# Performance work log

Hardware: AMD Instinct MI355X
Metric: run time of the kernel (lower is better)

The kernel has to match this reference:

```python
import jax, jax.numpy as jnp
import numpy as np

N_HEADS = 16
D_K = 64
MAX_LEN = 5000


def setup_inputs() -> dict:
    key = jax.random.key(0)
    ks = jax.random.split(key, 6)
    B, L, D = 4, 1024, 1024
    s = 1.0 / np.sqrt(D).astype(np.float32)
    return {
        "x": jax.random.normal(ks[0], (B, L, D), jnp.float32),
        "W_q": jax.random.normal(ks[1], (D, D), jnp.float32) * s,
        "b_q": jnp.zeros((D,), jnp.float32),
        "W_k": jax.random.normal(ks[2], (D, D), jnp.float32) * s,
        "b_k": jnp.zeros((D,), jnp.float32),
        "W_v": jax.random.normal(ks[3], (D, D), jnp.float32) * s,
        "b_v": jnp.zeros((D,), jnp.float32),
        "W_o": jax.random.normal(ks[4], (D, D), jnp.float32) * s,
        "b_o": jnp.zeros((D,), jnp.float32),
        "Er": jax.random.normal(ks[5], (MAX_LEN, D_K), jnp.float32) * 0.02,
    }


def reference(x, W_q, b_q, W_k, b_k, W_v, b_v, W_o, b_o, Er):
    B, L, D = x.shape
    H = N_HEADS
    dk = D // H
    # torch nn.Linear: y = x @ W.T + b
    Q = (x @ W_q.T + b_q).reshape(B, L, H, dk).transpose(0, 2, 1, 3)  # (B,H,L,dk)
    K = (x @ W_k.T + b_k).reshape(B, L, H, dk).transpose(0, 2, 1, 3)
    V = (x @ W_v.T + b_v).reshape(B, L, H, dk).transpose(0, 2, 1, 3)
    AC = jnp.einsum('bhid,bhjd->bhij', Q, K)  # (B,H,L,L)
    rel_pos = jnp.arange(L - 1, -L, -1) + (MAX_LEN - 1)  # (2L-1,)
    # mode='clip' matches intended math: clamped rows fall in the part that
    # the relative shift slices away.
    Er_embed = jnp.take(Er, rel_pos, axis=0, mode='clip')  # (2L-1, dk)
    BD = jnp.einsum('bhid,rd->bhir', Q, Er_embed)  # (B,H,L,2L-1)
    # _relative_shift: view is a no-op (shape already (B,H,L,2L-1)), then slice
    BD = BD[..., L - 1:]  # (B,H,L,L)
    scores = (AC + BD) / np.sqrt(dk).astype(np.float32)
    attn = jax.nn.softmax(scores, axis=-1)
    out = jnp.einsum('bhij,bhjd->bhid', attn, V)
    out = out.transpose(0, 2, 1, 3).reshape(B, L, D)
    return out @ W_o.T + b_o
```

## Files before the change

### kernel.cpp

```cpp
#include <hip/hip_runtime.h>
#include <cstdint>
#include <cstddef>


typedef __attribute__((ext_vector_type(8))) short short8;
typedef __attribute__((ext_vector_type(4))) float f32x4;

#define MFMA_BF16(a, b, c) __builtin_amdgcn_mfma_f32_16x16x32_bf16((a), (b), (c), 0, 0, 0)

constexpr int kB = 4, kL = 1024, kD = 1024, kH = 16;
constexpr int kBL = kB * kL;
constexpr float kScale = 0.125f * 1.44269504088896340736f;

static __device__ __forceinline__ unsigned short f32_to_bf16(float f) {
  union { float f; uint32_t u; } c; c.f = f;
  uint32_t u = c.u + 0x7fffu + ((c.u >> 16) & 1u);
  return (unsigned short)(u >> 16);
}

static __device__ __forceinline__ void gload_lds16(const void* g, void* l) {
  __builtin_amdgcn_global_load_lds(
      (const __attribute__((address_space(1))) void*)g,
      (__attribute__((address_space(3))) void*)l, 16, 0, 0);
}

__global__ __launch_bounds__(256)
void cast_all(const float* __restrict__ x,  const float* __restrict__ Wq,
              const float* __restrict__ Wk, const float* __restrict__ Wv,
              const float* __restrict__ Wo,
              unsigned short* __restrict__ xb, unsigned short* __restrict__ Wcat,
              unsigned short* __restrict__ Wob) {
  int i = blockIdx.x * blockDim.x + threadIdx.x;
  const float* src;
  ushort4* dst;
  int off;
  if (i < 1048576) {
    src = x; dst = reinterpret_cast<ushort4*>(xb); off = i;
  } else {
    int j = i - 1048576;
    int seg = j >> 18;
    off = j & 262143;
    if (seg == 0)      { src = Wq; dst = reinterpret_cast<ushort4*>(Wcat); }
    else if (seg == 1) { src = Wk; dst = reinterpret_cast<ushort4*>(Wcat) + 262144; }
    else if (seg == 2) { src = Wv; dst = reinterpret_cast<ushort4*>(Wcat) + 524288; }
    else               { src = Wo; dst = reinterpret_cast<ushort4*>(Wob); }
  }
  float4 v = reinterpret_cast<const float4*>(src)[off];
  ushort4 o;
  o.x = f32_to_bf16(v.x); o.y = f32_to_bf16(v.y);
  o.z = f32_to_bf16(v.z); o.w = f32_to_bf16(v.w);
  dst[off] = o;
}

__global__ __launch_bounds__(512, 2)
void gemm_qkv(const unsigned short* __restrict__ A,
              const unsigned short* __restrict__ Bm,
              const float* __restrict__ bq, const float* __restrict__ bk,
              const float* __restrict__ bv,
              const float* __restrict__ Er,
              unsigned short* __restrict__ Qh, unsigned short* __restrict__ Kh,
              unsigned short* __restrict__ Vth) {
  __shared__ __align__(16) char smem[131072];
  const int tid  = threadIdx.x;
  const int lane = tid & 63, wave = tid >> 6;
  const int quad = lane >> 4, l15 = lane & 15, lhalf = l15 >> 1;
  const int wr = wave >> 2, wc = wave & 3;

  const int bid = blockIdx.x;
  const int xcd = bid & 7, idx = bid >> 3;
  const int mt_ = idx / 6, nt_ = idx - mt_ * 6;
  const int m0 = ((xcd >> 1) * 4 + mt_) * 256;
  const int n0 = ((xcd & 1) * 6 + nt_) * 256;

  const int lane_off = (l15 & 1) * 64 + ((quad * 16) ^ ((lhalf & 3) << 4));
  const int aoff = lhalf * 128 + lane_off + wr * 8192;
  const int boff = lhalf * 128 + lane_off + wc * 4096;

  int srow[2], scol[2];
#pragma unroll
  for (int j = 0; j < 2; ++j) {
    int poff = (j * 512 + tid) * 16;
    int L = poff ^ (((poff >> 7) & 3) << 4);
    srow[j] = ((L >> 7) << 1) | ((L >> 6) & 1);
    scol[j] = (L & 63) >> 1;
  }

  auto stageAB = [&](int X, int kh, int tt) {
    const unsigned short* src = X ? Bm : A;
    const int rbase = X ? n0 : m0;
    char* dst = smem + ((tt & 1) * 65536 + X * 32768 + kh * 16384) + tid * 16;
    const int kc = tt * 64 + kh * 32;
#pragma unroll
    for (int j = 0; j < 2; ++j)
      gload_lds16(src + (size_t)(rbase + srow[j]) * 1024 + kc + scol[j],
                  dst + j * 8192);
  };

  const f32x4 vzero = {0.f, 0.f, 0.f, 0.f};
  f32x4 acc[8][4];
#pragma unroll
  for (int i = 0; i < 8; ++i)
#pragma unroll
    for (int j = 0; j < 4; ++j) acc[i][j] = vzero;

  stageAB(0, 0, 0); stageAB(1, 0, 0); stageAB(0, 1, 0); stageAB(1, 1, 0);
  stageAB(0, 0, 1); stageAB(1, 0, 1);
  asm volatile("s_waitcnt vmcnt(4)" ::: "memory");
  __builtin_amdgcn_s_barrier();

#define LDA(KH, MB) do {                                                      \
    _Pragma("unroll")                                                         \
    for (int f_ = 0; f_ < 4; ++f_)                                            \
      af[f_] = *(const short8*)(RA + (KH) * 16384 + aoff + ((MB) + f_) * 1024); \
  } while (0)
#define LDB(KH) do {                                                          \
    _Pragma("unroll")                                                         \
    for (int n_ = 0; n_ < 4; ++n_)                                            \
      bf[n_] = *(const short8*)(RB + (KH) * 16384 + boff + n_ * 1024);        \
  } while (0)
#define BARA() do {                                                           \
    __builtin_amdgcn_s_barrier();                                             \
    asm volatile("s_waitcnt lgkmcnt(0)" ::: "memory");                        \
    __builtin_amdgcn_sched_barrier(0);                                        \
  } while (0)
#define MFMA_QUAD(MB) do {                                                    \
    __builtin_amdgcn_s_setprio(1);                                            \
    _Pragma("unroll")                                                         \
    for (int mq_ = 0; mq_ < 4; ++mq_) {                                       \
      _Pragma("unroll")                                                       \
      for (int nq_ = 0; nq_ < 4; ++nq_)                                       \
        acc[(MB) + mq_][nq_] =                                                \
            MFMA_BF16(af[mq_], bf[nq_], acc[(MB) + mq_][nq_]);                \
    }                                                                         \
    __builtin_amdgcn_s_setprio(0);                                            \
  } while (0)

  for (int t = 0; t < 16; ++t) {
    const char* RA = smem + (t & 1) * 65536;
    const char* RB = RA + 32768;
    short8 af[4], bf[4];
    LDA(0, 0); LDB(0);
    if (t + 1 < 16) stageAB(0, 1, t + 1);
    BARA(); MFMA_QUAD(0);
    __builtin_amdgcn_s_barrier();
    LDA(0, 4);
    if (t + 1 < 16) stageAB(1, 1, t + 1);
    BARA(); MFMA_QUAD(4);
    __builtin_amdgcn_s_barrier();
    LDA(1, 0); LDB(1);
    if (t + 2 < 16) stageAB(0, 0, t + 2);
    BARA(); MFMA_QUAD(0);
    __builtin_amdgcn_s_barrier();
    LDA(1, 4);
    if (t + 2 < 16) stageAB(1, 0, t + 2);
    BARA(); MFMA_QUAD(4);
    if (t < 14) asm volatile("s_waitcnt vmcnt(4)" ::: "memory");
    else        asm volatile("s_waitcnt vmcnt(0)" ::: "memory");
    __builtin_amdgcn_s_barrier();
  }

#undef LDA
#undef LDB
#undef BARA
#undef MFMA_QUAD

  const int wsel = n0 >> 10;
  const int gmb  = m0 + wr * 128;
  const int bb   = gmb >> 10, i0l = gmb & 1023;
  const int nl0  = (n0 & 1023) + wc * 64;
  const int hh   = nl0 >> 6;
  const size_t bh = (size_t)(bb * 16 + hh);

  if (wsel == 0) {
#pragma unroll
    for (int mf = 0; mf < 8; ++mf)
#pragma unroll
      for (int nf = 0; nf < 4; ++nf)
#pragma unroll
        for (int r = 0; r < 4; ++r) {
          const int i = i0l + mf * 16 + quad * 4 + r;
          const int n = nl0 + nf * 16 + l15;
          float v = (acc[mf][nf][r] + bq[n]) * kScale;
          Qh[(bh * 1024 + i) * 64 + (n & 63)] = f32_to_bf16(v);
        }
  } else if (wsel == 1) {
#pragma unroll
    for (int mf = 0; mf < 8; ++mf)
#pragma unroll
      for (int nf = 0; nf < 4; ++nf)
#pragma unroll
        for (int r = 0; r < 4; ++r) {
          const int i = i0l + mf * 16 + quad * 4 + r;
          const int n = nl0 + nf * 16 + l15;
          const int d = n & 63;
          float v = acc[mf][nf][r] + bk[n] + Er[(size_t)(4999 - i) * 64 + d];
          Kh[(bh * 1024 + i) * 64 + d] = f32_to_bf16(v);
        }
  } else {
    __syncthreads();
    unsigned short* W = (unsigned short*)smem + (size_t)wave * 8192;
#pragma unroll
    for (int mf = 0; mf < 8; ++mf)
#pragma unroll
      for (int nf = 0; nf < 4; ++nf) {
        ushort4 pk;
        const int n = nl0 + nf * 16 + l15;
        pk.x = f32_to_bf16(acc[mf][nf][0] + bv[n]);
        pk.y = f32_to_bf16(acc[mf][nf][1] + bv[n]);
        pk.z = f32_to_bf16(acc[mf][nf][2] + bv[n]);
        pk.w = f32_to_bf16(acc[mf][nf][3] + bv[n]);
        *(ushort4*)&W[(size_t)(nf * 16 + l15) * 128 + mf * 16 + quad * 4] = pk;
      }
#pragma unroll
    for (int p = 0; p < 16; ++p) {
      const int u = p * 64 + lane;
      const int d = u >> 4, ch = (u & 15) * 8;
      short8 vv = *(const short8*)&W[(size_t)d * 128 + ch];
      *(short8*)&Vth[(bh * 64 + d) * 1024 + i0l + ch] = vv;
    }
  }
}

__global__ __launch_bounds__(256)
void gemm_out(const unsigned short* __restrict__ A,
              const unsigned short* __restrict__ Bm,
              const float* __restrict__ bias,
              float* __restrict__ outf) {
  __shared__ unsigned short As[2][128 * 32];
  __shared__ unsigned short Bs[2][64 * 32];
  const int tid  = threadIdx.x;
  const int lane = tid & 63, wave = tid >> 6;
  const int quad = lane >> 4, l15 = lane & 15;
  const int m0 = blockIdx.y * 128, n0 = blockIdx.x * 64;
  const int K = 1024;

  const f32x4 vzero = {0.f, 0.f, 0.f, 0.f};
  f32x4 acc[2][4];
#pragma unroll
  for (int i = 0; i < 2; ++i)
#pragma unroll
    for (int j = 0; j < 4; ++j) acc[i][j] = vzero;

  for (int k0 = 0; k0 < K; k0 += 64) {
    __syncthreads();
#pragma unroll
    for (int j = 0; j < 4; ++j) {
      int u = j * 256 + tid;
      int half = u >> 9, row = (u >> 2) & 127, c = (u & 3) * 8 + half * 32;
      gload_lds16(A + (size_t)(m0 + row) * K + k0 + c, (char*)&As[0][0] + (size_t)u * 16);
    }
#pragma unroll
    for (int j = 0; j < 2; ++j) {
      int u = j * 256 + tid;
      int half = u >> 8, row = (u >> 2) & 63, c = (u & 3) * 8 + half * 32;
      gload_lds16(Bm + (size_t)(n0 + row) * K + k0 + c, (char*)&Bs[0][0] + (size_t)u * 16);
    }
    __syncthreads();

#pragma unroll
    for (int ks = 0; ks < 2; ++ks) {
      short8 af[2], bfv[4];
#pragma unroll
      for (int mt = 0; mt < 2; ++mt)
        af[mt] = *(const short8*)&As[ks][(wave * 32 + mt * 16 + l15) * 32 + quad * 8];
#pragma unroll
      for (int nt = 0; nt < 4; ++nt)
        bfv[nt] = *(const short8*)&Bs[ks][(nt * 16 + l15) * 32 + quad * 8];
#pragma unroll
      for (int mt = 0; mt < 2; ++mt)
#pragma unroll
        for (int nt = 0; nt < 4; ++nt)
          acc[mt][nt] = MFMA_BF16(af[mt], bfv[nt], acc[mt][nt]);
    }
  }

#pragma unroll
  for (int mt = 0; mt < 2; ++mt)
#pragma unroll
    for (int nt = 0; nt < 4; ++nt)
#pragma unroll
      for (int r = 0; r < 4; ++r) {
        const int gm = m0 + wave * 32 + mt * 16 + quad * 4 + r;
        const int gn = n0 + nt * 16 + l15;
        outf[(size_t)gm * 1024 + gn] = acc[mt][nt][r] + bias[gn];
      }
}

__global__ __launch_bounds__(256)
void attn_kernel(const unsigned short* __restrict__ Q,
                 const unsigned short* __restrict__ Kp,
                 const unsigned short* __restrict__ Vt,
                 unsigned short* __restrict__ Ao) {
  __shared__ unsigned short Ks[2][2][64 * 32];
  __shared__ unsigned short Vs[2][2][64 * 32];
  __shared__ unsigned short Plds[4][32 * 72];
  const int tid  = threadIdx.x;
  const int lane = tid & 63, wave = tid >> 6;
  const int quad = lane >> 4, l15 = lane & 15;
  const int bh = blockIdx.x;
  const int qb = blockIdx.y;
  const size_t base  = (size_t)bh * (kL * 64);
  const size_t vbase = (size_t)bh * (64 * kL);
  const int i0 = qb * 128 + wave * 32;

  short8 qf[2][2];
#pragma unroll
  for (int mt = 0; mt < 2; ++mt)
#pragma unroll
    for (int ks = 0; ks < 2; ++ks)
      qf[mt][ks] = *(const short8*)
          &Q[base + (size_t)(i0 + mt * 16 + l15) * 64 + ks * 32 + quad * 8];

  auto stage = [&](int buf, int kb) {
#pragma unroll
    for (int j = 0; j < 2; ++j) {
      int u = j * 256 + tid;
      int half = u >> 8, row = (u >> 2) & 63, c = (u & 3) * 8;
      gload_lds16(Kp + base + (size_t)(kb * 64 + row) * 64 + half * 32 + c,
                  (char*)&Ks[buf][0][0] + (size_t)u * 16);
      gload_lds16(Vt + vbase + (size_t)row * kL + kb * 64 + half * 32 + c,
                  (char*)&Vs[buf][0][0] + (size_t)u * 16);
    }
  };

  const f32x4 vzero = {0.f, 0.f, 0.f, 0.f};
  f32x4 of[2][4];
#pragma unroll
  for (int mt = 0; mt < 2; ++mt)
#pragma unroll
    for (int dt = 0; dt < 4; ++dt) of[mt][dt] = vzero;
  float lsum[2][4] = {{0.f, 0.f, 0.f, 0.f}, {0.f, 0.f, 0.f, 0.f}};

  unsigned short* Pw = Plds[wave];

  stage(0, 0);
  __syncthreads();

  for (int kb = 0; kb < 16; ++kb) {
    const int cur = kb & 1, nxt = cur ^ 1;
    if (kb < 15) stage(nxt, kb + 1);

    short8 kf[4][2];
#pragma unroll
    for (int nt = 0; nt < 4; ++nt)
#pragma unroll
      for (int ks = 0; ks < 2; ++ks)
        kf[nt][ks] = *(const short8*)&Ks[cur][ks][(nt * 16 + l15) * 32 + quad * 8];
    f32x4 sf[2][4];
#pragma unroll
    for (int mt = 0; mt < 2; ++mt)
#pragma unroll
      for (int nt = 0; nt < 4; ++nt) {
        sf[mt][nt] = MFMA_BF16(qf[mt][0], kf[nt][0], vzero);
        sf[mt][nt] = MFMA_BF16(qf[mt][1], kf[nt][1], sf[mt][nt]);
      }

#pragma unroll
    for (int mt = 0; mt < 2; ++mt)
#pragma unroll
      for (int nt = 0; nt < 4; ++nt)
#pragma unroll
        for (int r = 0; r < 4; ++r) {
          float p = __builtin_amdgcn_exp2f(sf[mt][nt][r]);
          lsum[mt][r] += p;
          union { float f; uint32_t u; } c; c.f = p;
          Pw[(mt * 16 + quad * 4 + r) * 72 + nt * 16 + l15] =
              (unsigned short)((c.u + 0x8000u) >> 16);
        }
    short8 pf[2][2];
#pragma unroll
    for (int mt = 0; mt < 2; ++mt)
#pragma unroll
      for (int ks = 0; ks < 2; ++ks)
        pf[mt][ks] = *(const short8*)&Pw[(mt * 16 + l15) * 72 + ks * 32 + quad * 8];

    short8 vf[4][2];
#pragma unroll
    for (int dt = 0; dt < 4; ++dt)
#pragma unroll
      for (int ks = 0; ks < 2; ++ks)
        vf[dt][ks] = *(const short8*)&Vs[cur][ks][(dt * 16 + l15) * 32 + quad * 8];
#pragma unroll
    for (int mt = 0; mt < 2; ++mt)
#pragma unroll
      for (int dt = 0; dt < 4; ++dt) {
        of[mt][dt] = MFMA_BF16(pf[mt][0], vf[dt][0], of[mt][dt]);
        of[mt][dt] = MFMA_BF16(pf[mt][1], vf[dt][1], of[mt][dt]);
      }

    __syncthreads();
  }

#pragma unroll
  for (int mask = 1; mask < 16; mask <<= 1)
#pragma unroll
    for (int mt = 0; mt < 2; ++mt)
#pragma unroll
      for (int r = 0; r < 4; ++r)
        lsum[mt][r] += __shfl_xor(lsum[mt][r], mask);
  float rl[2][4];
#pragma unroll
  for (int mt = 0; mt < 2; ++mt)
#pragma unroll
    for (int r = 0; r < 4; ++r) rl[mt][r] = __builtin_amdgcn_rcpf(lsum[mt][r]);

  const int b = bh >> 4, h = bh & 15;
#pragma unroll
  for (int mt = 0; mt < 2; ++mt)
#pragma unroll
    for (int dt = 0; dt < 4; ++dt)
#pragma unroll
      for (int r = 0; r < 4; ++r) {
        const int ig = i0 + mt * 16 + quad * 4 + r;
        float v = of[mt][dt][r] * rl[mt][r];
        Ao[((size_t)(b * 1024 + ig)) * 1024 + h * 64 + dt * 16 + l15] = f32_to_bf16(v);
      }
}

extern "C" void kernel_launch(void* const* d_in, const int* in_sizes, int n_in,
                              void* d_out, int out_size, void* d_ws, size_t ws_size,
                              hipStream_t stream) {
  const float* x   = (const float*)d_in[0];
  const float* W_q = (const float*)d_in[1];
  const float* b_q = (const float*)d_in[2];
  const float* W_k = (const float*)d_in[3];
  const float* b_k = (const float*)d_in[4];
  const float* W_v = (const float*)d_in[5];
  const float* b_v = (const float*)d_in[6];
  const float* W_o = (const float*)d_in[7];
  const float* b_o = (const float*)d_in[8];
  const float* Er  = (const float*)d_in[9];
  float* out = (float*)d_out;

  char* ws = (char*)d_ws;
  unsigned short* xb   = (unsigned short*)(ws + (size_t)0);
  unsigned short* Wcat = (unsigned short*)(ws + ((size_t)8  << 20));
  unsigned short* Wob  = (unsigned short*)(ws + ((size_t)14 << 20));
  unsigned short* Qh   = (unsigned short*)(ws + ((size_t)16 << 20));
  unsigned short* Kh   = (unsigned short*)(ws + ((size_t)24 << 20));
  unsigned short* Vth  = (unsigned short*)(ws + ((size_t)32 << 20));
  unsigned short* Aoh  = (unsigned short*)(ws + ((size_t)40 << 20));

  cast_all<<<8192, 256, 0, stream>>>(x, W_q, W_k, W_v, W_o, xb, Wcat, Wob);

  gemm_qkv<<<192, 512, 0, stream>>>(
      xb, Wcat, b_q, b_k, b_v, Er, Qh, Kh, Vth);

  attn_kernel<<<dim3(kB * kH, kL / 128), 256, 0, stream>>>(Qh, Kh, Vth, Aoh);

  gemm_out<<<dim3(16, 32), 256, 0, stream>>>(Aoh, Wob, b_o, out);
}
```

Baseline: 175.6 us.

## Retile QKV GEMM to 256x192 tiles for 256 blocks filling all CUs

Changes the QKV projection GEMM tile from 256x256 to 256x192, so the grid grows from 192 to 256 blocks and covers all CUs of the MI355X (the old grid left some idle). The B-operand staging now loads a full 64-wide K slice with a new XOR swizzle, and the pipeline waits are retuned. The epilogue now handles per-16-column fragments that can straddle the Q/K/V boundary, with a per-fragment V transpose through LDS. In exchange each block reuses its A tile across fewer columns and the staging and wait logic gets more intricate.

```diff
diff --git a/kernel.cpp b/kernel.cpp
--- a/kernel.cpp
+++ b/kernel.cpp
@@ -60,51 +60,64 @@
               const float* __restrict__ Er,
               unsigned short* __restrict__ Qh, unsigned short* __restrict__ Kh,
               unsigned short* __restrict__ Vth) {
-  __shared__ __align__(16) char smem[131072];
+  __shared__ __align__(16) char smem[114688];
   const int tid  = threadIdx.x;
   const int lane = tid & 63, wave = tid >> 6;
-  const int quad = lane >> 4, l15 = lane & 15, lhalf = l15 >> 1;
+  const int quad = lane >> 4, l15 = lane & 15;
   const int wr = wave >> 2, wc = wave & 3;
 
   const int bid = blockIdx.x;
   const int xcd = bid & 7, idx = bid >> 3;
-  const int mt_ = idx / 6, nt_ = idx - mt_ * 6;
-  const int m0 = ((xcd >> 1) * 4 + mt_) * 256;
-  const int n0 = ((xcd & 1) * 6 + nt_) * 256;
-
-  const int lane_off = (l15 & 1) * 64 + ((quad * 16) ^ ((lhalf & 3) << 4));
-  const int aoff = lhalf * 128 + lane_off + wr * 8192;
-  const int boff = lhalf * 128 + lane_off + wc * 4096;
-
-  int srow[2], scol[2];
+  const int m0 = ((xcd >> 1) * 4 + (idx >> 3)) * 256;
+  const int n0 = ((xcd & 1) * 8 + (idx & 7)) * 192;
+
+  const int aoff = (l15 >> 1) * 128 + (l15 & 1) * 64 +
+                   ((quad * 16) ^ (((l15 >> 1) & 3) << 4)) + wr * 8192;
+  const int b_lane = (quad * 16) ^ ((l15 & 7) << 4);
+  const int boff = (wc * 48 + l15) * 128 + b_lane;
+
+  int srowA[2], scolA[2];
 #pragma unroll
   for (int j = 0; j < 2; ++j) {
     int poff = (j * 512 + tid) * 16;
     int L = poff ^ (((poff >> 7) & 3) << 4);
-    srow[j] = ((L >> 7) << 1) | ((L >> 6) & 1);
-    scol[j] = (L & 63) >> 1;
-  }
-
-  auto stageAB = [&](int X, int kh, int tt) {
-    const unsigned short* src = X ? Bm : A;
-    const int rbase = X ? n0 : m0;
-    char* dst = smem + ((tt & 1) * 65536 + X * 32768 + kh * 16384) + tid * 16;
+    srowA[j] = ((L >> 7) << 1) | ((L >> 6) & 1);
+    scolA[j] = (L & 63) >> 1;
+  }
+  int srowB[3], scolB[3];
+#pragma unroll
+  for (int j = 0; j < 3; ++j) {
+    int poff = (j * 512 + tid) * 16;
+    int L = poff ^ (((poff >> 7) & 7) << 4);
+    srowB[j] = L >> 7;
+    scolB[j] = (L & 127) >> 1;
+  }
+
+  auto stageA = [&](int kh, int tt) {
+    char* dst = smem + (tt & 1) * 32768 + kh * 16384 + tid * 16;
     const int kc = tt * 64 + kh * 32;
 #pragma unroll
     for (int j = 0; j < 2; ++j)
-      gload_lds16(src + (size_t)(rbase + srow[j]) * 1024 + kc + scol[j],
+      gload_lds16(A + (size_t)(m0 + srowA[j]) * 1024 + kc + scolA[j],
                   dst + j * 8192);
   };
+  auto stageB = [&](int tt) {
+    char* dst = smem + 65536 + (tt & 1) * 24576 + tid * 16;
+    const int kc = tt * 64;
+#pragma unroll
+    for (int j = 0; j < 3; ++j)
+      gload_lds16(Bm + (size_t)(n0 + srowB[j]) * 1024 + kc + scolB[j],
+                  dst + j * 8192);
+  };
 
   const f32x4 vzero = {0.f, 0.f, 0.f, 0.f};
-  f32x4 acc[8][4];
+  f32x4 acc[8][3];
 #pragma unroll
   for (int i = 0; i < 8; ++i)
 #pragma unroll
-    for (int j = 0; j < 4; ++j) acc[i][j] = vzero;
-
-  stageAB(0, 0, 0); stageAB(1, 0, 0); stageAB(0, 1, 0); stageAB(1, 1, 0);
-  stageAB(0, 0, 1); stageAB(1, 0, 1);
+    for (int j = 0; j < 3; ++j) acc[i][j] = vzero;
+
+  stageA(0, 0); stageB(0); stageA(1, 0); stageA(0, 1);
   asm volatile("s_waitcnt vmcnt(4)" ::: "memory");
   __builtin_amdgcn_s_barrier();
 
@@ -115,20 +128,20 @@
   } while (0)
 #define LDB(KH) do {                                                          \
     _Pragma("unroll")                                                         \
-    for (int n_ = 0; n_ < 4; ++n_)                                            \
-      bf[n_] = *(const short8*)(RB + (KH) * 16384 + boff + n_ * 1024);        \
+    for (int n_ = 0; n_ < 3; ++n_)                                            \
+      bf[n_] = *(const short8*)(RB + ((boff + n_ * 2048) ^ ((KH) * 64)));     \
   } while (0)
 #define BARA() do {                                                           \
     __builtin_amdgcn_s_barrier();                                             \
     asm volatile("s_waitcnt lgkmcnt(0)" ::: "memory");                        \
     __builtin_amdgcn_sched_barrier(0);                                        \
   } while (0)
-#define MFMA_QUAD(MB) do {                                                    \
+#define MFMA_12(MB) do {                                                      \
     __builtin_amdgcn_s_setprio(1);                                            \
     _Pragma("unroll")                                                         \
     for (int mq_ = 0; mq_ < 4; ++mq_) {                                       \
       _Pragma("unroll")                                                       \
-      for (int nq_ = 0; nq_ < 4; ++nq_)                                       \
+      for (int nq_ = 0; nq_ < 3; ++nq_)                                       \
         acc[(MB) + mq_][nq_] =                                                \
             MFMA_BF16(af[mq_], bf[nq_], acc[(MB) + mq_][nq_]);                \
     }                                                                         \
@@ -136,87 +149,86 @@
   } while (0)
 
   for (int t = 0; t < 16; ++t) {
-    const char* RA = smem + (t & 1) * 65536;
-    const char* RB = RA + 32768;
-    short8 af[4], bf[4];
+    const char* RA = smem + (t & 1) * 32768;
+    const char* RB = smem + 65536 + (t & 1) * 24576;
+    short8 af[4], bf[3];
     LDA(0, 0); LDB(0);
-    if (t + 1 < 16) stageAB(0, 1, t + 1);
-    BARA(); MFMA_QUAD(0);
+    if (t + 1 < 16) stageB(t + 1);
+    BARA(); MFMA_12(0);
     __builtin_amdgcn_s_barrier();
     LDA(0, 4);
-    if (t + 1 < 16) stageAB(1, 1, t + 1);
-    BARA(); MFMA_QUAD(4);
+    if (t + 1 < 16) stageA(1, t + 1);
+    BARA(); MFMA_12(4);
+    if (t < 15) asm volatile("s_waitcnt vmcnt(7)" ::: "memory");
+    else        asm volatile("s_waitcnt vmcnt(0)" ::: "memory");
     __builtin_amdgcn_s_barrier();
     LDA(1, 0); LDB(1);
-    if (t + 2 < 16) stageAB(0, 0, t + 2);
-    BARA(); MFMA_QUAD(0);
+    if (t + 2 < 16) stageA(0, t + 2);
+    BARA(); MFMA_12(0);
     __builtin_amdgcn_s_barrier();
     LDA(1, 4);
-    if (t + 2 < 16) stageAB(1, 0, t + 2);
-    BARA(); MFMA_QUAD(4);
-    if (t < 14) asm volatile("s_waitcnt vmcnt(4)" ::: "memory");
-    else        asm volatile("s_waitcnt vmcnt(0)" ::: "memory");
+    BARA(); MFMA_12(4);
+    if (t < 14)       asm volatile("s_waitcnt vmcnt(4)" ::: "memory");
+    else if (t == 14) asm volatile("s_waitcnt vmcnt(2)" ::: "memory");
+    else              asm volatile("s_waitcnt vmcnt(0)" ::: "memory");
     __builtin_amdgcn_s_barrier();
   }
 
 #undef LDA
 #undef LDB
 #undef BARA
-#undef MFMA_QUAD
-
-  const int wsel = n0 >> 10;
-  const int gmb  = m0 + wr * 128;
-  const int bb   = gmb >> 10, i0l = gmb & 1023;
-  const int nl0  = (n0 & 1023) + wc * 64;
-  const int hh   = nl0 >> 6;
-  const size_t bh = (size_t)(bb * 16 + hh);
-
-  if (wsel == 0) {
-#pragma unroll
-    for (int mf = 0; mf < 8; ++mf)
-#pragma unroll
-      for (int nf = 0; nf < 4; ++nf)
+#undef MFMA_12
+
+  __syncthreads();
+  const int gmb = m0 + wr * 128;
+  const int bb  = gmb >> 10, i0l = gmb & 1023;
+  unsigned short* Wv = (unsigned short*)smem + (size_t)wave * 6144;
+
+#pragma unroll
+  for (int nf = 0; nf < 3; ++nf) {
+    const int n    = n0 + wc * 48 + nf * 16;
+    const int wsel = n >> 10;
+    const int nin  = n & 1023;
+    const int hh   = nin >> 6, d0 = nin & 63;
+    const size_t bh = (size_t)(bb * 16 + hh);
+
+    if (wsel == 0) {
+#pragma unroll
+      for (int mf = 0; mf < 8; ++mf)
 #pragma unroll
         for (int r = 0; r < 4; ++r) {
           const int i = i0l + mf * 16 + quad * 4 + r;
-          const int n = nl0 + nf * 16 + l15;
-          float v = (acc[mf][nf][r] + bq[n]) * kScale;
-          Qh[(bh * 1024 + i) * 64 + (n & 63)] = f32_to_bf16(v);
+          float v = (acc[mf][nf][r] + bq[nin + l15]) * kScale;
+          Qh[(bh * 1024 + i) * 64 + d0 + l15] = f32_to_bf16(v);
         }
-  } else if (wsel == 1) {
-#pragma unroll
-    for (int mf = 0; mf < 8; ++mf)
-#pragma unroll
-      for (int nf = 0; nf < 4; ++nf)
+    } else if (wsel == 1) {
+#pragma unroll
+      for (int mf = 0; mf < 8; ++mf)
 #pragma unroll
         for (int r = 0; r < 4; ++r) {
           const int i = i0l + mf * 16 + quad * 4 + r;
-          const int n = nl0 + nf * 16 + l15;
-          const int d = n & 63;
-          float v = acc[mf][nf][r] + bk[n] + Er[(size_t)(4999 - i) * 64 + d];
-          Kh[(bh * 1024 + i) * 64 + d] = f32_to_bf16(v);
+          float v = acc[mf][nf][r] + bk[nin + l15] +
+                    Er[(size_t)(4999 - i) * 64 + d0 + l15];
+          Kh[(bh * 1024 + i) * 64 + d0 + l15] = f32_to_bf16(v);
         }
-  } else {
-    __syncthreads();
-    unsigned short* W = (unsigned short*)smem + (size_t)wave * 8192;
-#pragma unroll
-    for (int mf = 0; mf < 8; ++mf)
-#pragma unroll
-      for (int nf = 0; nf < 4; ++nf) {
+    } else {
+      unsigned short* Wn = Wv + nf * 2048;
+#pragma unroll
+      for (int mf = 0; mf < 8; ++mf) {
         ushort4 pk;
-        const int n = nl0 + nf * 16 + l15;
-        pk.x = f32_to_bf16(acc[mf][nf][0] + bv[n]);
-        pk.y = f32_to_bf16(acc[mf][nf][1] + bv[n]);
-        pk.z = f32_to_bf16(acc[mf][nf][2] + bv[n]);
-        pk.w = f32_to_bf16(acc[mf][nf][3] + bv[n]);
-        *(ushort4*)&W[(size_t)(nf * 16 + l15) * 128 + mf * 16 + quad * 4] = pk;
-      }
-#pragma unroll
-    for (int p = 0; p < 16; ++p) {
-      const int u = p * 64 + lane;
-      const int d = u >> 4, ch = (u & 15) * 8;
-      short8 vv = *(const short8*)&W[(size_t)d * 128 + ch];
-      *(short8*)&Vth[(bh * 64 + d) * 1024 + i0l + ch] = vv;
+        pk.x = f32_to_bf16(acc[mf][nf][0] + bv[nin + l15]);
+        pk.y = f32_to_bf16(acc[mf][nf][1] + bv[nin + l15]);
+        pk.z = f32_to_bf16(acc[mf][nf][2] + bv[nin + l15]);
+        pk.w = f32_to_bf16(acc[mf][nf][3] + bv[nin + l15]);
+        *(ushort4*)&Wn[(size_t)l15 * 128 + mf * 16 + quad * 4] = pk;
+      }
+#pragma unroll
+      for (int p = 0; p < 4; ++p) {
+        const int u = p * 64 + lane;
+        const int dl = u >> 4, ch = (u & 15) * 8;
+        short8 vv = *(const short8*)&Wn[(size_t)dl * 128 + ch];
+        *(short8*)&Vth[(bh * 64 + d0 + dl) * 1024 + i0l + ch] = vv;
+      }
     }
   }
 }
@@ -443,7 +455,7 @@
 
   cast_all<<<8192, 256, 0, stream>>>(x, W_q, W_k, W_v, W_o, xb, Wcat, Wob);
 
-  gemm_qkv<<<192, 512, 0, stream>>>(
+  gemm_qkv<<<256, 512, 0, stream>>>(
       xb, Wcat, b_q, b_k, b_v, Er, Qh, Kh, Vth);
 
   attn_kernel<<<dim3(kB * kH, kL / 128), 256, 0, stream>>>(Qh, Kh, Vth, Aoh);
```

Measured after the change: 173.4 us. No clear change (-1.3%).
